# Performance work log

Measured on AMD Instinct MI355X. Metric: run time of the kernel, lower is better.

## Reference

```python
import jax, jax.numpy as jnp
import numpy as np

VOCAB = 50000
DIM = 300
BATCH = 1024
CTX = 10


def setup_inputs() -> dict:
    key = jax.random.key(0)
    k1, k2, k3, k4 = jax.random.split(key, 4)
    context = jax.random.randint(k1, (BATCH, CTX), 0, VOCAB, dtype=jnp.int64 if jax.config.read('jax_enable_x64') else jnp.int32)
    W_proj = jax.random.normal(k2, (DIM, VOCAB), dtype=jnp.float32) * 0.02
    W_cls = jax.random.normal(k3, (VOCAB, DIM), dtype=jnp.float32) * 0.02
    b_cls = jax.random.normal(k4, (VOCAB,), dtype=jnp.float32) * 0.02
    return {"context": context, "W_proj": W_proj, "W_cls": W_cls, "b_cls": b_cls, "pad_idx": 0}


def reference(context, W_proj, W_cls, b_cls, pad_idx):
    # One-hot @ W_proj.T == gather of W_proj columns at context ids: [B, C, D]
    emb = jnp.take(W_proj, context, axis=1)            # [D, B, C]
    emb = jnp.moveaxis(emb, 0, -1)                     # [B, C, D]
    # zeroing the pad_idx column of the one-hot kills pad tokens' contribution,
    # but the mean still divides by the full context length C.
    mask = (context != pad_idx).astype(emb.dtype)      # [B, C]
    emb = emb * mask[..., None]
    pooled = emb.mean(axis=1)                          # [B, D]
    logits = pooled @ W_cls.T + b_cls                  # [B, V]
    return jax.nn.log_softmax(logits, axis=1)
```

## Files before the change

kernel.cpp:

```cpp
#include <hip/hip_runtime.h>
#include <math.h>

#define B_SZ 1024
#define CTXL 10
#define DIM  300
#define VOC  50000
#define KP   320
#define BM   128
#define BN   128
#define BK   64
#define NTIL 391
#define NSG  50
#define WROW 1200
#define WMAXOFF 59999984

typedef short s16x8 __attribute__((ext_vector_type(8)));
typedef float f32x4 __attribute__((ext_vector_type(4)));

__device__ __forceinline__ void gload_lds16(const void* g, void* lds) {
  __builtin_amdgcn_global_load_lds((const __attribute__((address_space(1))) void*)g,
                                   (__attribute__((address_space(3))) void*)lds, 16, 0, 0);
}

__global__ void transpose_kernel(const float* __restrict__ W, float* __restrict__ WT) {
  __shared__ float tile[32][33];
  const int v0 = blockIdx.x * 32, d0 = blockIdx.y * 32;
  const int tx = threadIdx.x & 31, ty = threadIdx.x >> 5;
#pragma unroll
  for (int i = 0; i < 32; i += 8) {
    const int d = d0 + ty + i, v = v0 + tx;
    tile[ty + i][tx] = (d < DIM && v < VOC) ? W[d * VOC + v] : 0.f;
  }
  __syncthreads();
#pragma unroll
  for (int i = 0; i < 32; i += 8) {
    const int v = v0 + ty + i, d = d0 + tx;
    if (v < VOC && d < DIM) WT[v * DIM + d] = tile[tx][ty + i];
  }
}

__global__ void pool_kernel(const int* __restrict__ ctx, const float* __restrict__ WT,
                            const int* __restrict__ padp, __bf16* __restrict__ pooled) {
  const int b = blockIdx.x;
  const int d = threadIdx.x;
  const int pad = *padp;
  float s = 0.f;
  if (d < DIM) {
#pragma unroll
    for (int c = 0; c < CTXL; ++c) {
      const int id = ctx[b * CTXL + c];
      if (id != pad) s += WT[id * DIM + d];
    }
  }
  pooled[b * KP + d] = (__bf16)(s * 0.1f);
}

__global__ __launch_bounds__(256, 2) void gemm_kernel(const __bf16* __restrict__ A,
                                                      const float* __restrict__ Wcls,
                                                      const float* __restrict__ bias,
                                                      float* __restrict__ out,
                                                      float* __restrict__ sumexp) {
  __shared__ __align__(16) char smem[65536];
  const int bid = blockIdx.x;
  const int s = bid & 7;
  const int mj = (bid >> 3) & 7;
  const int G = bid >> 6;
  const int nt = G * 8 + s;
  if (nt >= NTIL) return;
  const int m0 = mj * BM;
  const int n0 = nt * BN;
  const int t = threadIdx.x;
  const int lane = t & 63;
  const int wave = t >> 6;
  const int wm = wave >> 1, wn = wave & 1;

  f32x4 acc[4][4];
#pragma unroll
  for (int i = 0; i < 4; ++i)
#pragma unroll
    for (int j = 0; j < 4; ++j) acc[i][j] = (f32x4){0.f, 0.f, 0.f, 0.f};

  const char* Ab = (const char*)A;
  const char* Wb = (const char*)Wcls;
  const int hi = lane >> 4;
  const int lr8 = lane >> 3;
  const int gcA = (lane & 7) ^ lr8;
  const int brow = t >> 1;
  const int bhalf = t & 1;
  int browg = n0 + brow; if (browg > VOC - 1) browg = VOC - 1;

  {
#pragma unroll
    for (int i = 0; i < 4; ++i) {
      const int r = wave * 32 + i * 8 + lr8;
      gload_lds16(Ab + (m0 + r) * (KP * 2) + gcA * 16, smem + wave * 4096 + i * 1024);
    }
    f32x4 breg[8];
#pragma unroll
    for (int j = 0; j < 8; ++j) {
      int off = browg * WROW + (bhalf * 8 + j) * 16;
      if (off > WMAXOFF) off = WMAXOFF;
      breg[j] = *(const f32x4*)(Wb + off);
    }
#pragma unroll
    for (int jj = 0; jj < 4; ++jj) {
      union { __bf16 h; short v; } cv;
      s16x8 bb;
      cv.h = (__bf16)breg[jj * 2][0];     bb[0] = cv.v;
      cv.h = (__bf16)breg[jj * 2][1];     bb[1] = cv.v;
      cv.h = (__bf16)breg[jj * 2][2];     bb[2] = cv.v;
      cv.h = (__bf16)breg[jj * 2][3];     bb[3] = cv.v;
      cv.h = (__bf16)breg[jj * 2 + 1][0]; bb[4] = cv.v;
      cv.h = (__bf16)breg[jj * 2 + 1][1]; bb[5] = cv.v;
      cv.h = (__bf16)breg[jj * 2 + 1][2]; bb[6] = cv.v;
      cv.h = (__bf16)breg[jj * 2 + 1][3]; bb[7] = cv.v;
      const int c = bhalf * 4 + jj;
      *(s16x8*)(smem + 32768 + brow * 128 + ((c ^ (brow & 7)) * 16)) = bb;
    }
  }
  __syncthreads();

#pragma unroll
  for (int k = 0; k < 5; ++k) {
    char* bAc = smem + (k & 1) * 16384;
    char* bBc = smem + 32768 + (k & 1) * 16384;
    char* bAn = smem + ((k + 1) & 1) * 16384;
    char* bBn = smem + 32768 + ((k + 1) & 1) * 16384;

    f32x4 breg[8];
    if (k < 4) {
      const int k0n = (k + 1) * BK;
#pragma unroll
      for (int i = 0; i < 4; ++i) {
        const int r = wave * 32 + i * 8 + lr8;
        gload_lds16(Ab + (m0 + r) * (KP * 2) + k0n * 2 + gcA * 16, bAn + wave * 4096 + i * 1024);
      }
#pragma unroll
      for (int j = 0; j < 8; ++j) {
        int off = browg * WROW + (k0n / 4 + bhalf * 8 + j) * 16;
        if (off > WMAXOFF) off = WMAXOFF;
        breg[j] = *(const f32x4*)(Wb + off);
      }
    }

#pragma unroll
    for (int kk = 0; kk < 2; ++kk) {
      s16x8 af[4], bfr[4];
#pragma unroll
      for (int mf = 0; mf < 4; ++mf) {
        const int ra = wm * 64 + mf * 16 + (lane & 15);
        af[mf] = *(const s16x8*)(bAc + ra * 128 + (((kk * 4 + hi) ^ (ra & 7)) * 16));
      }
#pragma unroll
      for (int nf = 0; nf < 4; ++nf) {
        const int rb = wn * 64 + nf * 16 + (lane & 15);
        bfr[nf] = *(const s16x8*)(bBc + rb * 128 + (((kk * 4 + hi) ^ (rb & 7)) * 16));
      }
#pragma unroll
      for (int mf = 0; mf < 4; ++mf)
#pragma unroll
        for (int nf = 0; nf < 4; ++nf)
          acc[mf][nf] = __builtin_amdgcn_mfma_f32_16x16x32_bf16(af[mf], bfr[nf], acc[mf][nf], 0, 0, 0);
    }

    if (k < 4) {
#pragma unroll
      for (int jj = 0; jj < 4; ++jj) {
        union { __bf16 h; short v; } cv;
        s16x8 bb;
        cv.h = (__bf16)breg[jj * 2][0];     bb[0] = cv.v;
        cv.h = (__bf16)breg[jj * 2][1];     bb[1] = cv.v;
        cv.h = (__bf16)breg[jj * 2][2];     bb[2] = cv.v;
        cv.h = (__bf16)breg[jj * 2][3];     bb[3] = cv.v;
        cv.h = (__bf16)breg[jj * 2 + 1][0]; bb[4] = cv.v;
        cv.h = (__bf16)breg[jj * 2 + 1][1]; bb[5] = cv.v;
        cv.h = (__bf16)breg[jj * 2 + 1][2]; bb[6] = cv.v;
        cv.h = (__bf16)breg[jj * 2 + 1][3]; bb[7] = cv.v;
        const int c = bhalf * 4 + jj;
        *(s16x8*)(bBn + brow * 128 + ((c ^ (brow & 7)) * 16)) = bb;
      }
    }
    __syncthreads();
  }

  const int cl = lane & 15, lg = lane >> 4;
#pragma unroll
  for (int mf = 0; mf < 4; ++mf) {
    float rs[4] = {0.f, 0.f, 0.f, 0.f};
#pragma unroll
    for (int nf = 0; nf < 4; ++nf) {
      const int col = n0 + wn * 64 + nf * 16 + cl;
      const bool valid = col < VOC;
      const float bia = valid ? bias[col] : -1e30f;
#pragma unroll
      for (int reg = 0; reg < 4; ++reg) {
        const int row = m0 + wm * 64 + mf * 16 + lg * 4 + reg;
        const float logit = acc[mf][nf][reg] + bia;
        if (valid) out[row * VOC + col] = logit;
        rs[reg] += __expf(logit);
      }
    }
#pragma unroll
    for (int reg = 0; reg < 4; ++reg) {
      float v = rs[reg];
      v += __shfl_xor(v, 1, 16);
      v += __shfl_xor(v, 2, 16);
      v += __shfl_xor(v, 4, 16);
      v += __shfl_xor(v, 8, 16);
      if (cl == 0) {
        const int row = m0 + wm * 64 + mf * 16 + lg * 4 + reg;
        atomicAdd(&sumexp[row], v);
      }
    }
  }
}

__global__ void lse_kernel(const float* __restrict__ sumexp, float* __restrict__ lse) {
  const int b = blockIdx.x * blockDim.x + threadIdx.x;
  if (b < B_SZ) lse[b] = logf(sumexp[b]);
}

__global__ void finalize_kernel(float* __restrict__ out, const float* __restrict__ lse) {
  const int i = blockIdx.x * 256 + threadIdx.x;
  const int b = blockIdx.y;
  if (i < VOC / 4) {
    const float l = lse[b];
    float4* p = (float4*)out + b * (VOC / 4) + i;
    float4 v = *p;
    v.x -= l; v.y -= l; v.z -= l; v.w -= l;
    *p = v;
  }
}

extern "C" void kernel_launch(void* const* d_in, const int* in_sizes, int n_in,
                              void* d_out, int out_size, void* d_ws, size_t ws_size,
                              hipStream_t stream) {
  (void)in_sizes; (void)n_in; (void)out_size;
  const int*   ctx   = (const int*)d_in[0];
  const float* Wproj = (const float*)d_in[1];
  const float* Wcls  = (const float*)d_in[2];
  const float* bcls  = (const float*)d_in[3];
  const int*   padp  = (const int*)d_in[4];
  float* out = (float*)d_out;

  if (ws_size < 663552) return;
  char* ws = (char*)d_ws;
  __bf16* pooled = (__bf16*)ws;
  float*  sumexp = (float*)(ws + 655360);
  float*  lse    = (float*)(ws + 655360 + 4096);
  float*  WT     = out;

  hipMemsetAsync(sumexp, 0, B_SZ * sizeof(float), stream);
  transpose_kernel<<<dim3(1563, 10), 256, 0, stream>>>(Wproj, WT);
  pool_kernel<<<B_SZ, KP, 0, stream>>>(ctx, WT, padp, pooled);
  gemm_kernel<<<NSG * 64, 256, 0, stream>>>(pooled, Wcls, bcls, out, sumexp);
  lse_kernel<<<4, 256, 0, stream>>>(sumexp, lse);
  finalize_kernel<<<dim3(49, B_SZ), 256, 0, stream>>>(out, lse);
}
```

Before: 526.0 us.

## Move softmax sum out of GEMM into fused per-row softfix kernel

The GEMM epilogue no longer computes exp sums or issues atomics. It only writes logits plus bias, and the B tile becomes single-buffered so shared memory drops to 48KB, allowing three blocks per CU. A new per-row kernel reads each logit row once, stashes it in shared memory as fp16, reduces the exp sum, and writes log-softmax back. This replaces the memset, lse and finalize kernels. The fp16 stash loses precision on the final outputs, and the single B buffer adds an extra barrier per k-step.

Result: faster. 480.9 us (-8.6%).

```diff
diff --git a/kernel.cpp b/kernel.cpp
--- a/kernel.cpp
+++ b/kernel.cpp
@@ -16,6 +16,7 @@
 
 typedef short s16x8 __attribute__((ext_vector_type(8)));
 typedef float f32x4 __attribute__((ext_vector_type(4)));
+typedef _Float16 h4 __attribute__((ext_vector_type(4)));
 
 __device__ __forceinline__ void gload_lds16(const void* g, void* lds) {
   __builtin_amdgcn_global_load_lds((const __attribute__((address_space(1))) void*)g,
@@ -55,12 +56,11 @@
   pooled[b * KP + d] = (__bf16)(s * 0.1f);
 }
 
-__global__ __launch_bounds__(256, 2) void gemm_kernel(const __bf16* __restrict__ A,
+__global__ __launch_bounds__(256, 3) void gemm_kernel(const __bf16* __restrict__ A,
                                                       const float* __restrict__ Wcls,
                                                       const float* __restrict__ bias,
-                                                      float* __restrict__ out,
-                                                      float* __restrict__ sumexp) {
-  __shared__ __align__(16) char smem[65536];
+                                                      float* __restrict__ out) {
+  __shared__ __align__(16) char smem[49152];
   const int bid = blockIdx.x;
   const int s = bid & 7;
   const int mj = (bid >> 3) & 7;
@@ -82,23 +82,26 @@
 
   const char* Ab = (const char*)A;
   const char* Wb = (const char*)Wcls;
+  char* bufA[2] = {smem, smem + 16384};
+  char* bufB = smem + 32768;
   const int hi = lane >> 4;
   const int lr8 = lane >> 3;
   const int gcA = (lane & 7) ^ lr8;
   const int brow = t >> 1;
   const int bhalf = t & 1;
   int browg = n0 + brow; if (browg > VOC - 1) browg = VOC - 1;
-
+  const long browoff = (long)browg * WROW;
+
+#pragma unroll
+  for (int i = 0; i < 4; ++i) {
+    const int r = wave * 32 + i * 8 + lr8;
+    gload_lds16(Ab + (m0 + r) * (KP * 2) + gcA * 16, bufA[0] + wave * 4096 + i * 1024);
+  }
   {
-#pragma unroll
-    for (int i = 0; i < 4; ++i) {
-      const int r = wave * 32 + i * 8 + lr8;
-      gload_lds16(Ab + (m0 + r) * (KP * 2) + gcA * 16, smem + wave * 4096 + i * 1024);
-    }
     f32x4 breg[8];
 #pragma unroll
     for (int j = 0; j < 8; ++j) {
-      int off = browg * WROW + (bhalf * 8 + j) * 16;
+      long off = browoff + (bhalf * 8 + j) * 16;
       if (off > WMAXOFF) off = WMAXOFF;
       breg[j] = *(const f32x4*)(Wb + off);
     }
@@ -115,17 +118,15 @@
       cv.h = (__bf16)breg[jj * 2 + 1][2]; bb[6] = cv.v;
       cv.h = (__bf16)breg[jj * 2 + 1][3]; bb[7] = cv.v;
       const int c = bhalf * 4 + jj;
-      *(s16x8*)(smem + 32768 + brow * 128 + ((c ^ (brow & 7)) * 16)) = bb;
+      *(s16x8*)(bufB + brow * 128 + ((c ^ (brow & 7)) * 16)) = bb;
     }
   }
   __syncthreads();
 
 #pragma unroll
   for (int k = 0; k < 5; ++k) {
-    char* bAc = smem + (k & 1) * 16384;
-    char* bBc = smem + 32768 + (k & 1) * 16384;
-    char* bAn = smem + ((k + 1) & 1) * 16384;
-    char* bBn = smem + 32768 + ((k + 1) & 1) * 16384;
+    char* bAc = bufA[k & 1];
+    char* bAn = bufA[(k + 1) & 1];
 
     f32x4 breg[8];
     if (k < 4) {
@@ -137,7 +138,7 @@
       }
 #pragma unroll
       for (int j = 0; j < 8; ++j) {
-        int off = browg * WROW + (k0n / 4 + bhalf * 8 + j) * 16;
+        long off = browoff + (k0n / 4 + bhalf * 8 + j) * 16;
         if (off > WMAXOFF) off = WMAXOFF;
         breg[j] = *(const f32x4*)(Wb + off);
       }
@@ -154,7 +155,7 @@
 #pragma unroll
       for (int nf = 0; nf < 4; ++nf) {
         const int rb = wn * 64 + nf * 16 + (lane & 15);
-        bfr[nf] = *(const s16x8*)(bBc + rb * 128 + (((kk * 4 + hi) ^ (rb & 7)) * 16));
+        bfr[nf] = *(const s16x8*)(bufB + rb * 128 + (((kk * 4 + hi) ^ (rb & 7)) * 16));
       }
 #pragma unroll
       for (int mf = 0; mf < 4; ++mf)
@@ -164,6 +165,7 @@
     }
 
     if (k < 4) {
+      __syncthreads();
 #pragma unroll
       for (int jj = 0; jj < 4; ++jj) {
         union { __bf16 h; short v; } cv;
@@ -177,58 +179,61 @@
         cv.h = (__bf16)breg[jj * 2 + 1][2]; bb[6] = cv.v;
         cv.h = (__bf16)breg[jj * 2 + 1][3]; bb[7] = cv.v;
         const int c = bhalf * 4 + jj;
-        *(s16x8*)(bBn + brow * 128 + ((c ^ (brow & 7)) * 16)) = bb;
-      }
-    }
-    __syncthreads();
+        *(s16x8*)(bufB + brow * 128 + ((c ^ (brow & 7)) * 16)) = bb;
+      }
+      __syncthreads();
+    }
   }
 
   const int cl = lane & 15, lg = lane >> 4;
 #pragma unroll
-  for (int mf = 0; mf < 4; ++mf) {
-    float rs[4] = {0.f, 0.f, 0.f, 0.f};
-#pragma unroll
-    for (int nf = 0; nf < 4; ++nf) {
-      const int col = n0 + wn * 64 + nf * 16 + cl;
-      const bool valid = col < VOC;
-      const float bia = valid ? bias[col] : -1e30f;
-#pragma unroll
-      for (int reg = 0; reg < 4; ++reg) {
-        const int row = m0 + wm * 64 + mf * 16 + lg * 4 + reg;
-        const float logit = acc[mf][nf][reg] + bia;
-        if (valid) out[row * VOC + col] = logit;
-        rs[reg] += __expf(logit);
-      }
-    }
-#pragma unroll
-    for (int reg = 0; reg < 4; ++reg) {
-      float v = rs[reg];
-      v += __shfl_xor(v, 1, 16);
-      v += __shfl_xor(v, 2, 16);
-      v += __shfl_xor(v, 4, 16);
-      v += __shfl_xor(v, 8, 16);
-      if (cl == 0) {
-        const int row = m0 + wm * 64 + mf * 16 + lg * 4 + reg;
-        atomicAdd(&sumexp[row], v);
-      }
-    }
-  }
-}
-
-__global__ void lse_kernel(const float* __restrict__ sumexp, float* __restrict__ lse) {
-  const int b = blockIdx.x * blockDim.x + threadIdx.x;
-  if (b < B_SZ) lse[b] = logf(sumexp[b]);
-}
-
-__global__ void finalize_kernel(float* __restrict__ out, const float* __restrict__ lse) {
-  const int i = blockIdx.x * 256 + threadIdx.x;
-  const int b = blockIdx.y;
-  if (i < VOC / 4) {
-    const float l = lse[b];
-    float4* p = (float4*)out + b * (VOC / 4) + i;
-    float4 v = *p;
-    v.x -= l; v.y -= l; v.z -= l; v.w -= l;
-    *p = v;
+  for (int nf = 0; nf < 4; ++nf) {
+    const int col = n0 + wn * 64 + nf * 16 + cl;
+    if (col < VOC) {
+      const float bia = bias[col];
+#pragma unroll
+      for (int mf = 0; mf < 4; ++mf)
+#pragma unroll
+        for (int reg = 0; reg < 4; ++reg) {
+          const int row = m0 + wm * 64 + mf * 16 + lg * 4 + reg;
+          out[row * VOC + col] = acc[mf][nf][reg] + bia;
+        }
+    }
+  }
+}
+
+__global__ __launch_bounds__(1024) void softfix_kernel(float* __restrict__ out) {
+  extern __shared__ __align__(16) char stash[];
+  __shared__ float red[17];
+  const int b = blockIdx.x;
+  const int tid = threadIdx.x;
+  float4* rowp = (float4*)(out + b * VOC);
+  h4* st = (h4*)stash;
+
+  float s = 0.f;
+  for (int i = tid; i < VOC / 4; i += 1024) {
+    const float4 v = rowp[i];
+    h4 h;
+    h[0] = (_Float16)v.x; h[1] = (_Float16)v.y;
+    h[2] = (_Float16)v.z; h[3] = (_Float16)v.w;
+    st[i] = h;
+    s += __expf(v.x) + __expf(v.y) + __expf(v.z) + __expf(v.w);
+  }
+#pragma unroll
+  for (int off = 1; off < 64; off <<= 1) s += __shfl_xor(s, off, 64);
+  if ((tid & 63) == 0) red[tid >> 6] = s;
+  __syncthreads();
+  float tot = 0.f;
+#pragma unroll
+  for (int j = 0; j < 16; ++j) tot += red[j];
+  const float l = logf(tot);
+
+  for (int i = tid; i < VOC / 4; i += 1024) {
+    const h4 h = st[i];
+    float4 o;
+    o.x = (float)h[0] - l; o.y = (float)h[1] - l;
+    o.z = (float)h[2] - l; o.w = (float)h[3] - l;
+    rowp[i] = o;
   }
 }
 
@@ -243,17 +248,12 @@
   const int*   padp  = (const int*)d_in[4];
   float* out = (float*)d_out;
 
-  if (ws_size < 663552) return;
-  char* ws = (char*)d_ws;
-  __bf16* pooled = (__bf16*)ws;
-  float*  sumexp = (float*)(ws + 655360);
-  float*  lse    = (float*)(ws + 655360 + 4096);
+  if (ws_size < 655360) return;
+  __bf16* pooled = (__bf16*)d_ws;
   float*  WT     = out;
 
-  hipMemsetAsync(sumexp, 0, B_SZ * sizeof(float), stream);
   transpose_kernel<<<dim3(1563, 10), 256, 0, stream>>>(Wproj, WT);
   pool_kernel<<<B_SZ, KP, 0, stream>>>(ctx, WT, padp, pooled);
-  gemm_kernel<<<NSG * 64, 256, 0, stream>>>(pooled, Wcls, bcls, out, sumexp);
-  lse_kernel<<<4, 256, 0, stream>>>(sumexp, lse);
-  finalize_kernel<<<dim3(49, B_SZ), 256, 0, stream>>>(out, lse);
-}
+  gemm_kernel<<<NSG * 64, 256, 0, stream>>>(pooled, Wcls, bcls, out);
+  softfix_kernel<<<B_SZ, 1024, 100352, stream>>>(out);
+}
```
